# Kernel optimization log

Measured on AMD Instinct MI355X. Metric: run time of the kernel, lower is better.

Reference implementation:

```python
import jax, jax.numpy as jnp
import numpy as np


def _conv3x3(x, w):
    # x: [B,Cin,H,W], w: [Cout,Cin,3,3], stride 1, pad 1
    return jax.lax.conv_general_dilated(x, w, window_strides=(1, 1), padding='SAME',
                                        dimension_numbers=('NCHW', 'OIHW', 'NCHW'))


def _affine(x, s, b):
    # per-channel folded eval-mode BatchNorm (+ absorbed conv bias)
    return x * s[None, :, None, None] + b[None, :, None, None]


def _lif_encode(h, thr, beta, T=4):
    # LIF integrate-and-fire scan: membrane = beta*m + h; STE spike; soft reset.
    def step(m, _):
        m = beta * m + h
        sig = jax.nn.sigmoid(4.0 * (m - thr))
        hard = (m > thr).astype(h.dtype)
        spk = sig + jax.lax.stop_gradient(hard - sig)  # surrogate-gradient STE
        return m - spk * thr, spk
    _, spikes = jax.lax.scan(step, jnp.zeros_like(h), None, length=T)
    return spikes  # [T,B,C_bot,H,W]


def _level(feat, ew, ebs, ebb, thr, braw, dw, dbs, dbb):
    h = _affine(_conv3x3(feat, ew), ebs, ebb)
    spikes = _lif_encode(h, thr, jax.nn.sigmoid(braw))
    avg = spikes.mean(axis=0)  # ber=0.0 -> BSC channel is identity
    return jax.nn.silu(_affine(_conv3x3(avg, dw), dbs, dbb))


def _forward(feat3, enc3_w, enc3_bn_s, enc3_bn_b, enc3_thr, enc3_beta_raw, dec3_w, dec3_bn_s, dec3_bn_b,
             feat4, enc4_w, enc4_bn_s, enc4_bn_b, enc4_thr, enc4_beta_raw, dec4_w, dec4_bn_s, dec4_bn_b,
             feat5, enc5_w, enc5_bn_s, enc5_bn_b, enc5_thr, enc5_beta_raw, dec5_w, dec5_bn_s, dec5_bn_b):
    r3 = _level(feat3, enc3_w, enc3_bn_s, enc3_bn_b, enc3_thr, enc3_beta_raw, dec3_w, dec3_bn_s, dec3_bn_b)
    r4 = _level(feat4, enc4_w, enc4_bn_s, enc4_bn_b, enc4_thr, enc4_beta_raw, dec4_w, dec4_bn_s, dec4_bn_b)
    r5 = _level(feat5, enc5_w, enc5_bn_s, enc5_bn_b, enc5_thr, enc5_beta_raw, dec5_w, dec5_bn_s, dec5_bn_b)
    return (r3, r4, r5)


def setup_inputs() -> dict:
    key = jax.random.key(0)
    C_bot, B = 36, 16
    levels = {3: (64, 160), 4: (128, 80), 5: (256, 40)}
    inp = {}
    k = key
    for lvl, (c, s) in levels.items():
        k, k1, k2, k3 = jax.random.split(k, 4)
        inp[f'feat{lvl}'] = jax.random.normal(k1, (B, c, s, s), jnp.float32)
        inp[f'enc{lvl}_w'] = jax.random.normal(k2, (C_bot, c, 3, 3), jnp.float32) / np.float32(np.sqrt(9 * c))
        inp[f'enc{lvl}_bn_s'] = jnp.ones((C_bot,), jnp.float32)
        inp[f'enc{lvl}_bn_b'] = jnp.zeros((C_bot,), jnp.float32)
        inp[f'enc{lvl}_thr'] = jnp.ones((1, C_bot, 1, 1), jnp.float32)
        inp[f'enc{lvl}_beta_raw'] = jnp.full((1, C_bot, 1, 1), 2.2, jnp.float32)
        inp[f'dec{lvl}_w'] = jax.random.normal(k3, (c, C_bot, 3, 3), jnp.float32) / np.float32(np.sqrt(9 * C_bot))
        inp[f'dec{lvl}_bn_s'] = jnp.ones((c,), jnp.float32)
        inp[f'dec{lvl}_bn_b'] = jnp.zeros((c,), jnp.float32)
    return inp


def reference(feat3, enc3_w, enc3_bn_s, enc3_bn_b, enc3_thr, enc3_beta_raw, dec3_w, dec3_bn_s, dec3_bn_b,
              feat4, enc4_w, enc4_bn_s, enc4_bn_b, enc4_thr, enc4_beta_raw, dec4_w, dec4_bn_s, dec4_bn_b,
              feat5, enc5_w, enc5_bn_s, enc5_bn_b, enc5_thr, enc5_beta_raw, dec5_w, dec5_bn_s, dec5_bn_b):
    return _forward(feat3, enc3_w, enc3_bn_s, enc3_bn_b, enc3_thr, enc3_beta_raw, dec3_w, dec3_bn_s, dec3_bn_b,
                    feat4, enc4_w, enc4_bn_s, enc4_bn_b, enc4_thr, enc4_beta_raw, dec4_w, dec4_bn_s, dec4_bn_b,
                    feat5, enc5_w, enc5_bn_s, enc5_bn_b, enc5_thr, enc5_beta_raw, dec5_w, dec5_bn_s, dec5_bn_b)
```

## Files before the change

kernel.cpp:

```cpp
#include <hip/hip_runtime.h>
#include <hip/hip_bf16.h>

typedef __attribute__((ext_vector_type(8)))  short short8v;
typedef __attribute__((ext_vector_type(16))) float f32x16;
typedef __attribute__((ext_vector_type(4)))  int   int4v;

template<int CIN>
__global__ __launch_bounds__(256) void pack_we(
    const float* __restrict__ w, __hip_bfloat16* __restrict__ whi,
    __hip_bfloat16* __restrict__ wlo, int total)
{
    const int NCHUNK = CIN / 16;
    int idx = blockIdx.x * 256 + threadIdx.x;
    if (idx >= total) return;
    int m  = idx & 31;
    int h  = (idx >> 5) & 1;
    int s  = (idx >> 6) % 9;
    int c  = (idx / 576) % NCHUNK;
    int cg = idx / (576 * NCHUNK);
    int co = cg * 32 + m;
    unsigned short vh[8], vl[8];
    #pragma unroll
    for (int j = 0; j < 8; ++j) {
        int ci = c * 16 + h * 8 + j;
        float x = (co < 36) ? w[(long)co * CIN * 9 + ci * 9 + s] : 0.f;
        __hip_bfloat16 xh = __float2bfloat16(x);
        float rem = x - __bfloat162float(xh);
        __hip_bfloat16 xl = __float2bfloat16(rem);
        vh[j] = *(unsigned short*)&xh;
        vl[j] = *(unsigned short*)&xl;
    }
    *(int4v*)(whi + (long)idx * 8) = *(int4v*)vh;
    *(int4v*)(wlo + (long)idx * 8) = *(int4v*)vl;
}

template<int CIN, int PXB>
__global__ __launch_bounds__(256) void feat_hl(
    const float* __restrict__ f, __hip_bfloat16* __restrict__ fhl,
    int HW, int npx)
{
    const int NCHUNK = CIN / 16;
    __shared__ float t[CIN][PXB];
    const int p0 = blockIdx.x * PXB;

    for (int i = threadIdx.x; i < CIN * PXB; i += 256) {
        int ci = i / PXB, px = i % PXB;
        int p = p0 + px;
        float v = 0.f;
        if (p < npx) {
            int b = p / HW, r = p - b * HW;
            v = f[((long)b * CIN + ci) * HW + r];
        }
        t[ci][px] = v;
    }
    __syncthreads();

    for (int i = threadIdx.x; i < PXB * NCHUNK * 4; i += 256) {
        int q  = i & 3;
        int px = (i >> 2) % PXB;
        int c  = i / (4 * PXB);
        int p = p0 + px;
        if (p >= npx) continue;
        const bool lo = (q >= 2);
        const int ch0 = c * 16 + (q & 1) * 8;
        unsigned short v[8];
        #pragma unroll
        for (int j = 0; j < 8; ++j) {
            float x = t[ch0 + j][px];
            __hip_bfloat16 xh = __float2bfloat16(x);
            if (lo) {
                float rem = x - __bfloat162float(xh);
                xh = __float2bfloat16(rem);
            }
            v[j] = *(unsigned short*)&xh;
        }
        *(int4v*)(fhl + ((long)c * npx + p) * 32 + q * 8) = *(int4v*)v;
    }
}

template<int CIN>
__global__ __launch_bounds__(256) void enc_mfma_cl(
    const __hip_bfloat16* __restrict__ fhl,
    const __hip_bfloat16* __restrict__ whi,
    const __hip_bfloat16* __restrict__ wlo,
    const float* __restrict__ bn_s, const float* __restrict__ bn_b,
    const float* __restrict__ thr, const float* __restrict__ beta_raw,
    __hip_bfloat16* __restrict__ avg,
    int H, int W, int tiles_x)
{
    const int NCHUNK = CIN / 16;
    __shared__ __align__(16) short sbuf[324 * 48];
    short* hi_t = sbuf;
    short* lo_t = sbuf + 324 * 24;

    const int tid = threadIdx.x;
    const int b   = blockIdx.y;
    const int tx0 = (blockIdx.x % tiles_x) * 16;
    const int ty0 = (blockIdx.x / tiles_x) * 16;
    const long npx = (long)16 * H * W;

    const int lane = tid & 63;
    const int wv   = tid >> 6;
    const int h    = lane >> 5;
    const int n    = lane & 31;
    const int lx   = n & 15;
    const int ly0  = wv * 4 + (n >> 4);

    f32x16 acc[2][2];
    #pragma unroll
    for (int cg = 0; cg < 2; ++cg)
        #pragma unroll
        for (int pf = 0; pf < 2; ++pf)
            #pragma unroll
            for (int k = 0; k < 16; ++k) acc[cg][pf][k] = 0.f;

    const char* aph = (const char*)whi + h * 512 + n * 16;
    const char* apl = (const char*)wlo + h * 512 + n * 16;
    const long  cgstride = (long)NCHUNK * 9216;

    for (int c = 0; c < NCHUNK; ++c) {
        for (int i = tid; i < 1296; i += 256) {
            int p = i >> 2, q = i & 3;
            int hy = p / 18, hx = p - hy * 18;
            int gy = ty0 + hy - 1, gx = tx0 + hx - 1;
            int4v v = {0, 0, 0, 0};
            if (gy >= 0 && gy < H && gx >= 0 && gx < W) {
                long pg = (long)(b * H + gy) * W + gx;
                v = *(const int4v*)(fhl + ((long)c * npx + pg) * 32 + q * 8);
            }
            char* dst = (q < 2) ? (char*)hi_t + p * 48 + q * 16
                                : (char*)lo_t + p * 48 + (q - 2) * 16;
            *(int4v*)dst = v;
        }
        __syncthreads();

        const char* ahc = aph + (long)c * 9216;
        const char* alc = apl + (long)c * 9216;
        #pragma unroll
        for (int s = 0; s < 9; ++s) {
            const int dy = s / 3, dx = s % 3;
            const int p0 = (ly0 + dy) * 18 + (lx + dx);
            const int p1 = p0 + 36;
            short8v bh0 = *(const short8v*)((const char*)hi_t + p0 * 48 + h * 16);
            short8v bh1 = *(const short8v*)((const char*)hi_t + p1 * 48 + h * 16);
            short8v bl0 = *(const short8v*)((const char*)lo_t + p0 * 48 + h * 16);
            short8v bl1 = *(const short8v*)((const char*)lo_t + p1 * 48 + h * 16);
            #pragma unroll
            for (int cg = 0; cg < 2; ++cg) {
                short8v af = *(const short8v*)(ahc + cg * cgstride + s * 1024);
                short8v al = *(const short8v*)(alc + cg * cgstride + s * 1024);
                acc[cg][0] = __builtin_amdgcn_mfma_f32_32x32x16_bf16(af, bh0, acc[cg][0], 0, 0, 0);
                acc[cg][0] = __builtin_amdgcn_mfma_f32_32x32x16_bf16(af, bl0, acc[cg][0], 0, 0, 0);
                acc[cg][0] = __builtin_amdgcn_mfma_f32_32x32x16_bf16(al, bh0, acc[cg][0], 0, 0, 0);
                acc[cg][1] = __builtin_amdgcn_mfma_f32_32x32x16_bf16(af, bh1, acc[cg][1], 0, 0, 0);
                acc[cg][1] = __builtin_amdgcn_mfma_f32_32x32x16_bf16(af, bl1, acc[cg][1], 0, 0, 0);
                acc[cg][1] = __builtin_amdgcn_mfma_f32_32x32x16_bf16(al, bh1, acc[cg][1], 0, 0, 0);
            }
        }
        __syncthreads();
    }

    for (int i = tid; i < 1280; i += 256)
        *(int4v*)((char*)sbuf + i * 16) = (int4v){0, 0, 0, 0};
    __syncthreads();

    #pragma unroll
    for (int cg = 0; cg < 2; ++cg) {
        #pragma unroll
        for (int r = 0; r < 16; ++r) {
            const int co = (cg << 5) + (r & 3) + ((r >> 2) << 3) + (h << 2);
            if (co < 36) {
                const float sc   = bn_s[co], sb = bn_b[co];
                const float beta = 1.f / (1.f + expf(-beta_raw[co]));
                const float t    = thr[co];
                #pragma unroll
                for (int pf = 0; pf < 2; ++pf) {
                    const int ly = ly0 + pf * 2;
                    float hv = acc[cg][pf][r] * sc + sb;
                    float m = 0.f, c2 = 0.f;
                    #pragma unroll
                    for (int s4 = 0; s4 < 4; ++s4) {
                        m = beta * m + hv;
                        if (m > t) { c2 += 1.f; m -= t; }
                    }
                    __hip_bfloat16 ov = __float2bfloat16(c2 * 0.25f);
                    sbuf[(ly * 16 + lx) * 40 + co] = *(short*)&ov;
                }
            }
        }
    }
    __syncthreads();

    const long tilebase = ((long)(b * H + ty0) * W + tx0) * 40;
    for (int i = tid; i < 1280; i += 256) {
        int px = i / 5, u = i - px * 5;
        int py2 = px >> 4, px2 = px & 15;
        *(int4v*)(avg + tilebase + ((long)py2 * W + px2) * 40 + u * 8) =
            *(const int4v*)(sbuf + px * 40 + u * 8);
    }
}

template<int CIN, int CIPER>
__global__ __launch_bounds__(256) void enc_mfma_p(
    const __hip_bfloat16* __restrict__ fhl,
    const __hip_bfloat16* __restrict__ whi,
    const __hip_bfloat16* __restrict__ wlo,
    float* __restrict__ partial,
    int H, int W, int tiles_x)
{
    const int NCH_TOT = CIN / 16;
    const int NCH_PER = CIPER / 16;
    __shared__ __align__(16) short sbuf[324 * 48];
    short* hi_t = sbuf;
    short* lo_t = sbuf + 324 * 24;

    const int tid = threadIdx.x;
    const int b   = blockIdx.y;
    const int cis = blockIdx.z;
    const int tx0 = (blockIdx.x % tiles_x) * 16;
    const int ty0 = (blockIdx.x / tiles_x) * 16;
    const long npx = (long)16 * H * W;

    const int lane = tid & 63;
    const int wv   = tid >> 6;
    const int h    = lane >> 5;
    const int n    = lane & 31;
    const int lx   = n & 15;
    const int ly0  = wv * 4 + (n >> 4);

    f32x16 acc[2][2];
    #pragma unroll
    for (int cg = 0; cg < 2; ++cg)
        #pragma unroll
        for (int pf = 0; pf < 2; ++pf)
            #pragma unroll
            for (int k = 0; k < 16; ++k) acc[cg][pf][k] = 0.f;

    const char* aph = (const char*)whi + h * 512 + n * 16;
    const char* apl = (const char*)wlo + h * 512 + n * 16;
    const long  cgstride = (long)NCH_TOT * 9216;

    for (int c = 0; c < NCH_PER; ++c) {
        const int gc = cis * NCH_PER + c;
        for (int i = tid; i < 1296; i += 256) {
            int p = i >> 2, q = i & 3;
            int hy = p / 18, hx = p - hy * 18;
            int gy = ty0 + hy - 1, gx = tx0 + hx - 1;
            int4v v = {0, 0, 0, 0};
            if (gy >= 0 && gy < H && gx >= 0 && gx < W) {
                long pg = (long)(b * H + gy) * W + gx;
                v = *(const int4v*)(fhl + ((long)gc * npx + pg) * 32 + q * 8);
            }
            char* dst = (q < 2) ? (char*)hi_t + p * 48 + q * 16
                                : (char*)lo_t + p * 48 + (q - 2) * 16;
            *(int4v*)dst = v;
        }
        __syncthreads();

        const char* ahc = aph + (long)gc * 9216;
        const char* alc = apl + (long)gc * 9216;
        #pragma unroll
        for (int s = 0; s < 9; ++s) {
            const int dy = s / 3, dx = s % 3;
            const int p0 = (ly0 + dy) * 18 + (lx + dx);
            const int p1 = p0 + 36;
            short8v bh0 = *(const short8v*)((const char*)hi_t + p0 * 48 + h * 16);
            short8v bh1 = *(const short8v*)((const char*)hi_t + p1 * 48 + h * 16);
            short8v bl0 = *(const short8v*)((const char*)lo_t + p0 * 48 + h * 16);
            short8v bl1 = *(const short8v*)((const char*)lo_t + p1 * 48 + h * 16);
            #pragma unroll
            for (int cg = 0; cg < 2; ++cg) {
                short8v af = *(const short8v*)(ahc + cg * cgstride + s * 1024);
                short8v al = *(const short8v*)(alc + cg * cgstride + s * 1024);
                acc[cg][0] = __builtin_amdgcn_mfma_f32_32x32x16_bf16(af, bh0, acc[cg][0], 0, 0, 0);
                acc[cg][0] = __builtin_amdgcn_mfma_f32_32x32x16_bf16(af, bl0, acc[cg][0], 0, 0, 0);
                acc[cg][0] = __builtin_amdgcn_mfma_f32_32x32x16_bf16(al, bh0, acc[cg][0], 0, 0, 0);
                acc[cg][1] = __builtin_amdgcn_mfma_f32_32x32x16_bf16(af, bh1, acc[cg][1], 0, 0, 0);
                acc[cg][1] = __builtin_amdgcn_mfma_f32_32x32x16_bf16(af, bl1, acc[cg][1], 0, 0, 0);
                acc[cg][1] = __builtin_amdgcn_mfma_f32_32x32x16_bf16(al, bh1, acc[cg][1], 0, 0, 0);
            }
        }
        __syncthreads();
    }

    const int HW = H * W;
    const long total = (long)16 * 36 * HW;
    #pragma unroll
    for (int cg = 0; cg < 2; ++cg) {
        #pragma unroll
        for (int r = 0; r < 16; ++r) {
            const int co = (cg << 5) + (r & 3) + ((r >> 2) << 3) + (h << 2);
            if (co < 36) {
                #pragma unroll
                for (int pf = 0; pf < 2; ++pf) {
                    const int gy = ty0 + ly0 + pf * 2, gx = tx0 + lx;
                    if (gy < H && gx < W)
                        partial[(long)cis * total + ((long)(b * 36 + co) * HW + gy * W + gx)]
                            = acc[cg][pf][r];
                }
            }
        }
    }
}

template<int CIN, int CIPER, int CICHUNK, int COCHUNK, int TDIM, bool PARTIAL, bool CL>
__global__ __launch_bounds__(TDIM* TDIM) void enc_tiled(
    const float* __restrict__ feat,
    const float* __restrict__ w,
    const float* __restrict__ bn_s, const float* __restrict__ bn_b,
    const float* __restrict__ thr, const float* __restrict__ beta_raw,
    __hip_bfloat16* __restrict__ avg,
    float* __restrict__ partial,
    int H, int W, int tiles_x)
{
    const int TPB  = TDIM * TDIM;
    const int HALOD = TDIM + 2;
    const int NCO  = 36 / COCHUNK;
    __shared__ float fs[CICHUNK][HALOD][HALOD];

    const int tile = blockIdx.x;
    const int b    = blockIdx.y;
    const int coc  = blockIdx.z % NCO;
    const int cis  = blockIdx.z / NCO;
    const int co0  = coc * COCHUNK;
    const int tx0  = (tile % tiles_x) * TDIM;
    const int ty0  = (tile / tiles_x) * TDIM;

    const int tx = threadIdx.x % TDIM;
    const int ty = threadIdx.x / TDIM;
    const int ox = tx0 + tx, oy = ty0 + ty;

    float acc[COCHUNK];
    #pragma unroll
    for (int c = 0; c < COCHUNK; ++c) acc[c] = 0.f;

    const float* fb = feat + (long)b * CIN * H * W;
    const int ci_base = cis * CIPER;

    for (int cc = ci_base; cc < ci_base + CIPER; cc += CICHUNK) {
        for (int i = threadIdx.x; i < CICHUNK * HALOD * HALOD; i += TPB) {
            int ci = i / (HALOD * HALOD);
            int r  = i % (HALOD * HALOD);
            int hy = r / HALOD, hx = r % HALOD;
            int gy = ty0 + hy - 1, gx = tx0 + hx - 1;
            float v = 0.f;
            if (gy >= 0 && gy < H && gx >= 0 && gx < W)
                v = fb[((long)(cc + ci) * H + gy) * W + gx];
            fs[ci][hy][hx] = v;
        }
        __syncthreads();

        for (int ci = 0; ci < CICHUNK; ++ci) {
            float f0 = fs[ci][ty    ][tx], f1 = fs[ci][ty    ][tx+1], f2 = fs[ci][ty    ][tx+2];
            float f3 = fs[ci][ty + 1][tx], f4 = fs[ci][ty + 1][tx+1], f5 = fs[ci][ty + 1][tx+2];
            float f6 = fs[ci][ty + 2][tx], f7 = fs[ci][ty + 2][tx+1], f8 = fs[ci][ty + 2][tx+2];
            const float* wq = w + (long)(cc + ci) * 9;
            #pragma unroll
            for (int j = 0; j < COCHUNK; ++j) {
                const float* ww = wq + (long)(co0 + j) * CIN * 9;
                acc[j] += f0 * ww[0] + f1 * ww[1] + f2 * ww[2]
                        + f3 * ww[3] + f4 * ww[4] + f5 * ww[5]
                        + f6 * ww[6] + f7 * ww[7] + f8 * ww[8];
            }
        }
        __syncthreads();
    }

    if (ox < W && oy < H) {
        if (PARTIAL) {
            #pragma unroll
            for (int j = 0; j < COCHUNK; ++j)
                partial[((((long)cis * 16 + b) * 36 + (co0 + j)) * H + oy) * W + ox] = acc[j];
        } else {
            float cnt[COCHUNK];
            #pragma unroll
            for (int j = 0; j < COCHUNK; ++j) {
                int co = co0 + j;
                float hh   = acc[j] * bn_s[co] + bn_b[co];
                float beta = 1.f / (1.f + expf(-beta_raw[co]));
                float t    = thr[co];
                float m = 0.f, c2 = 0.f;
                #pragma unroll
                for (int s = 0; s < 4; ++s) {
                    m = beta * m + hh;
                    if (m > t) { c2 += 1.f; m -= t; }
                }
                cnt[j] = c2 * 0.25f;
            }
            if (CL) {
                unsigned* dp = (unsigned*)(avg + ((long)(b * H + oy) * W + ox) * 40 + co0);
                #pragma unroll
                for (int j2 = 0; j2 < COCHUNK / 2; ++j2) {
                    __hip_bfloat16 h0 = __float2bfloat16(cnt[2 * j2]);
                    __hip_bfloat16 h1 = __float2bfloat16(cnt[2 * j2 + 1]);
                    unsigned u0 = *(unsigned short*)&h0;
                    unsigned u1 = *(unsigned short*)&h1;
                    dp[j2] = u0 | (u1 << 16);
                }
            } else {
                #pragma unroll
                for (int j = 0; j < COCHUNK; ++j)
                    avg[(((long)b * 36 + (co0 + j)) * H + oy) * W + ox] = __float2bfloat16(cnt[j]);
            }
        }
    }
}

template<int SPLITS, bool CL>
__global__ __launch_bounds__(256) void combine_lif(
    const float* __restrict__ partial,
    const float* __restrict__ bn_s, const float* __restrict__ bn_b,
    const float* __restrict__ thr, const float* __restrict__ beta_raw,
    __hip_bfloat16* __restrict__ avg, int H, int W, int total)
{
    int idx = blockIdx.x * 256 + threadIdx.x;
    if (idx >= total) return;
    int HW = H * W;
    int co = (idx / HW) % 36;
    float hh = 0.f;
    #pragma unroll
    for (int s = 0; s < SPLITS; ++s) hh += partial[(long)s * total + idx];
    hh = hh * bn_s[co] + bn_b[co];
    float beta = 1.f / (1.f + expf(-beta_raw[co]));
    float t    = thr[co];
    float m = 0.f, cnt = 0.f;
    #pragma unroll
    for (int s = 0; s < 4; ++s) {
        m = beta * m + hh;
        if (m > t) { cnt += 1.f; m -= t; }
    }
    if (CL) {
        int b = idx / (36 * HW);
        int rem = idx % HW;
        int y = rem / W, x = rem % W;
        avg[((long)(b * H + y) * W + x) * 40 + co] = __float2bfloat16(cnt * 0.25f);
    } else {
        avg[idx] = __float2bfloat16(cnt * 0.25f);
    }
}

__global__ __launch_bounds__(256) void pack_w(
    const float* __restrict__ w, __hip_bfloat16* __restrict__ ap, int total)
{
    int idx = blockIdx.x * 256 + threadIdx.x;
    if (idx >= total) return;
    int m  = idx & 31;
    int h  = (idx >> 5) & 1;
    int s  = (idx >> 6) % 23;
    int cg = idx / (23 * 64);
    int o  = 2 * s + h;
    int co = cg * 32 + m;
    unsigned short v[8];
    #pragma unroll
    for (int j = 0; j < 8; ++j) {
        float x = 0.f;
        if (o < 45) {
            int tap = o / 5, oct = o % 5, ci = oct * 8 + j;
            if (ci < 36) x = w[(long)co * 324 + ci * 9 + tap];
        }
        __hip_bfloat16 hv = __float2bfloat16(x);
        v[j] = *(unsigned short*)&hv;
    }
    *(int4v*)(ap + (long)idx * 8) = *(int4v*)v;
}

template<int COG>
__global__ __launch_bounds__(256) void dec_mfma(
    const __hip_bfloat16* __restrict__ avg_cl,
    const __hip_bfloat16* __restrict__ apack,
    const float* __restrict__ bn_s, const float* __restrict__ bn_b,
    float* __restrict__ out, int Cout, int H, int W, int tiles_x)
{
    __shared__ __hip_bfloat16 tile[12960];

    const int tid    = threadIdx.x;
    const int b      = blockIdx.y;
    const int cgbase = blockIdx.z * COG;
    const int tx0 = (blockIdx.x % tiles_x) * 16;
    const int ty0 = (blockIdx.x / tiles_x) * 16;

    {
        const __hip_bfloat16* ab = avg_cl + (long)b * H * W * 40;
        for (int i = tid; i < 1620; i += 256) {
            int row = i / 90, u = i - row * 90;
            int px = u / 5, un = u - px * 5;
            int gy = ty0 + row - 1, gx = tx0 + px - 1;
            int4v v = {0, 0, 0, 0};
            if (gy >= 0 && gy < H && gx >= 0 && gx < W)
                v = *(const int4v*)(ab + ((long)gy * W + gx) * 40 + un * 8);
            *(int4v*)(tile + (row * 18 + px) * 40 + un * 8) = v;
        }
    }
    __syncthreads();

    const int lane = tid & 63;
    const int wv   = tid >> 6;
    const int h    = lane >> 5;
    const int n    = lane & 31;
    const int lx   = n & 15;
    const int ly0  = wv * 4 + (n >> 4);

    const char* tb  = (const char*)tile;
    const int   bb0 = ((ly0 + 1) * 18 + (lx + 1)) * 80;
    const int   bb1 = bb0 + 2 * 18 * 80;

    const char* ap = (const char*)apack + (long)cgbase * 23552 + h * 512 + n * 16;

    f32x16 acc[COG][2];
    #pragma unroll
    for (int cg = 0; cg < COG; ++cg)
        #pragma unroll
        for (int pf = 0; pf < 2; ++pf)
            #pragma unroll
            for (int k = 0; k < 16; ++k) acc[cg][pf][k] = 0.f;

    #pragma unroll
    for (int s = 0; s < 23; ++s) {
        int o0 = 2 * s;     if (o0 > 44) o0 = 44;
        int o1 = 2 * s + 1; if (o1 > 44) o1 = 44;
        const int C0 = ((o0 / 5) / 3 - 1) * 1440 + ((o0 / 5) % 3 - 1) * 80 + (o0 % 5) * 16;
        const int C1 = ((o1 / 5) / 3 - 1) * 1440 + ((o1 / 5) % 3 - 1) * 80 + (o1 % 5) * 16;
        const int offc = h ? C1 : C0;
        short8v bf0 = *(const short8v*)(tb + (bb0 + offc));
        short8v bf1 = *(const short8v*)(tb + (bb1 + offc));
        #pragma unroll
        for (int cg = 0; cg < COG; ++cg) {
            short8v af = *(const short8v*)(ap + cg * 23552 + s * 1024);
            acc[cg][0] = __builtin_amdgcn_mfma_f32_32x32x16_bf16(af, bf0, acc[cg][0], 0, 0, 0);
            acc[cg][1] = __builtin_amdgcn_mfma_f32_32x32x16_bf16(af, bf1, acc[cg][1], 0, 0, 0);
        }
    }

    #pragma unroll
    for (int cg = 0; cg < COG; ++cg) {
        #pragma unroll
        for (int r = 0; r < 16; ++r) {
            const int co = ((cgbase + cg) << 5) + (r & 3) + ((r >> 2) << 3) + (h << 2);
            const float sc = bn_s[co], bc = bn_b[co];
            #pragma unroll
            for (int pf = 0; pf < 2; ++pf) {
                const int ly = ly0 + pf * 2;
                const int gy = ty0 + ly, gx = tx0 + lx;
                float v = acc[cg][pf][r] * sc + bc;
                v = v / (1.f + __expf(-v));
                if (gy < H && gx < W)
                    out[(((long)b * Cout + co) * H + gy) * W + gx] = v;
            }
        }
    }
}

template<int COCHUNK, int TDIM>
__global__ __launch_bounds__(TDIM* TDIM) void dec_tiled(
    const __hip_bfloat16* __restrict__ avg,
    const float* __restrict__ w,
    const float* __restrict__ bn_s, const float* __restrict__ bn_b,
    float* __restrict__ out,
    int Cout, int H, int W, int tiles_x)
{
    const int CIN = 36;
    const int TPB = TDIM * TDIM;
    const int HALOD = TDIM + 2;
    __shared__ float fs[CIN][HALOD][HALOD];

    const int tile = blockIdx.x;
    const int b    = blockIdx.y;
    const int co0  = blockIdx.z * COCHUNK;
    const int tx0  = (tile % tiles_x) * TDIM;
    const int ty0  = (tile / tiles_x) * TDIM;

    const int tx = threadIdx.x % TDIM;
    const int ty = threadIdx.x / TDIM;
    const int ox = tx0 + tx, oy = ty0 + ty;

    const __hip_bfloat16* ab = avg + (long)b * CIN * H * W;

    for (int i = threadIdx.x; i < CIN * HALOD * HALOD; i += TPB) {
        int ci = i / (HALOD * HALOD);
        int r  = i % (HALOD * HALOD);
        int hy = r / HALOD, hx = r % HALOD;
        int gy = ty0 + hy - 1, gx = tx0 + hx - 1;
        float v = 0.f;
        if (gy >= 0 && gy < H && gx >= 0 && gx < W)
            v = __bfloat162float(ab[((long)ci * H + gy) * W + gx]);
        fs[ci][hy][hx] = v;
    }
    __syncthreads();

    float acc[COCHUNK];
    #pragma unroll
    for (int j = 0; j < COCHUNK; ++j) acc[j] = 0.f;

    for (int ci = 0; ci < CIN; ++ci) {
        float f0 = fs[ci][ty    ][tx], f1 = fs[ci][ty    ][tx+1], f2 = fs[ci][ty    ][tx+2];
        float f3 = fs[ci][ty + 1][tx], f4 = fs[ci][ty + 1][tx+1], f5 = fs[ci][ty + 1][tx+2];
        float f6 = fs[ci][ty + 2][tx], f7 = fs[ci][ty + 2][tx+1], f8 = fs[ci][ty + 2][tx+2];
        #pragma unroll
        for (int j = 0; j < COCHUNK; ++j) {
            const float* ww = w + ((long)(co0 + j) * CIN + ci) * 9;
            acc[j] += f0 * ww[0] + f1 * ww[1] + f2 * ww[2]
                    + f3 * ww[3] + f4 * ww[4] + f5 * ww[5]
                    + f6 * ww[6] + f7 * ww[7] + f8 * ww[8];
        }
    }

    if (ox < W && oy < H) {
        #pragma unroll
        for (int j = 0; j < COCHUNK; ++j) {
            int co = co0 + j;
            float v = acc[j] * bn_s[co] + bn_b[co];
            out[(((long)b * Cout + co) * H + oy) * W + ox] = v / (1.f + expf(-v));
        }
    }
}

extern "C" void kernel_launch(void* const* d_in, const int* in_sizes, int n_in,
                              void* d_out, int out_size, void* d_ws, size_t ws_size,
                              hipStream_t stream)
{
    const int B = 16;
    const int C[3] = {64, 128, 256};
    const int S[3] = {160, 80, 40};

    float* out = (float*)d_out;
    long out_off[3]; long off = 0;
    for (int l = 0; l < 3; ++l) { out_off[l] = off; off += (long)B * C[l] * S[l] * S[l]; }

    const long avgcl_bytes[3] = {32768000L, 8192000L, 2048000L};
    long avgcl_off[3]; long boff = 0;
    for (int l = 0; l < 3; ++l) { avgcl_off[l] = boff; boff += avgcl_bytes[l]; }
    const long avgcl_total = boff;
    const long ap_bytes[3] = {47104L, 94208L, 188416L};
    long ap_off[3];
    for (int l = 0; l < 3; ++l) { ap_off[l] = boff; boff += ap_bytes[l]; }
    const long we_bytes[3] = {73728L, 147456L, 294912L};
    long wehi_off[3], welo_off[3];
    for (int l = 0; l < 3; ++l) { wehi_off[l] = boff; boff += we_bytes[l];
                                  welo_off[l] = boff; boff += we_bytes[l]; }
    const long part5_off = boff;
    const long part5_bytes = 4L * B * 36 * 1600 * 4;
    boff += part5_bytes;
    const size_t need_full = (size_t)boff;
    const size_t need_min  = (size_t)part5_off;
    const long fhl_bytes[3] = {104857600L, 52428800L, 26214400L};
    long fhl_off[3];
    for (int l = 0; l < 2; ++l) { fhl_off[l] = boff; boff += fhl_bytes[l]; }
    const size_t need_cl = (size_t)boff;
    fhl_off[2] = boff; boff += fhl_bytes[2];
    const size_t need_cl5 = (size_t)boff;

    char* wsb = (char*)d_ws;

    if (ws_size >= need_min) {
        const bool split5  = ws_size >= need_full;
        const bool use_cl  = ws_size >= need_cl;
        const bool use_cl5 = ws_size >= need_cl5;
        hipMemsetAsync(wsb, 0, avgcl_total, stream);

        for (int l = 0; l < 3; ++l) {
            const float* dec_w = (const float*)d_in[9 * l + 6];
            int total = (C[l] / 32) * 23 * 2 * 32;
            pack_w<<<(total + 255) / 256, 256, 0, stream>>>(
                dec_w, (__hip_bfloat16*)(wsb + ap_off[l]), total);
        }
        {
            const float* enc_w3 = (const float*)d_in[1];
            int total = 2 * (64 / 16) * 9 * 2 * 32;
            pack_we<64><<<(total + 255) / 256, 256, 0, stream>>>(
                enc_w3, (__hip_bfloat16*)(wsb + wehi_off[0]),
                (__hip_bfloat16*)(wsb + welo_off[0]), total);
        }
        {
            const float* enc_w4 = (const float*)d_in[10];
            int total = 2 * (128 / 16) * 9 * 2 * 32;
            pack_we<128><<<(total + 255) / 256, 256, 0, stream>>>(
                enc_w4, (__hip_bfloat16*)(wsb + wehi_off[1]),
                (__hip_bfloat16*)(wsb + welo_off[1]), total);
        }
        if (use_cl5) {
            const float* enc_w5 = (const float*)d_in[19];
            int total = 2 * (256 / 16) * 9 * 2 * 32;
            pack_we<256><<<(total + 255) / 256, 256, 0, stream>>>(
                enc_w5, (__hip_bfloat16*)(wsb + wehi_off[2]),
                (__hip_bfloat16*)(wsb + welo_off[2]), total);
        }
        if (use_cl) {
            {
                int HW = 160 * 160, npx = B * HW;
                feat_hl<64, 64><<<(npx + 63) / 64, 256, 0, stream>>>(
                    (const float*)d_in[0], (__hip_bfloat16*)(wsb + fhl_off[0]), HW, npx);
            }
            {
                int HW = 80 * 80, npx = B * HW;
                feat_hl<128, 64><<<(npx + 63) / 64, 256, 0, stream>>>(
                    (const float*)d_in[9], (__hip_bfloat16*)(wsb + fhl_off[1]), HW, npx);
            }
        }
        if (use_cl5) {
            int HW = 40 * 40, npx = B * HW;
            feat_hl<256, 32><<<(npx + 31) / 32, 256, 0, stream>>>(
                (const float*)d_in[18], (__hip_bfloat16*)(wsb + fhl_off[2]), HW, npx);
        }

        for (int l = 0; l < 3; ++l) {
            const int base = 9 * l;
            const float* feat     = (const float*)d_in[base + 0];
            const float* enc_w    = (const float*)d_in[base + 1];
            const float* enc_bn_s = (const float*)d_in[base + 2];
            const float* enc_bn_b = (const float*)d_in[base + 3];
            const float* enc_thr  = (const float*)d_in[base + 4];
            const float* enc_beta = (const float*)d_in[base + 5];
            const float* dec_bn_s = (const float*)d_in[base + 7];
            const float* dec_bn_b = (const float*)d_in[base + 8];

            const int Hs = S[l], Wsz = S[l];
            __hip_bfloat16* avg_cl = (__hip_bfloat16*)(wsb + avgcl_off[l]);
            const __hip_bfloat16* ap = (const __hip_bfloat16*)(wsb + ap_off[l]);
            float* r = out + out_off[l];

            if (l == 0) {
                dim3 eg(100, B);
                if (use_cl)
                    enc_mfma_cl<64><<<eg, 256, 0, stream>>>(
                        (const __hip_bfloat16*)(wsb + fhl_off[0]),
                        (const __hip_bfloat16*)(wsb + wehi_off[0]),
                        (const __hip_bfloat16*)(wsb + welo_off[0]),
                        enc_bn_s, enc_bn_b, enc_thr, enc_beta, avg_cl, Hs, Wsz, 10);
                else
                    enc_tiled<64, 64, 16, 12, 16, false, true><<<dim3(100, B, 3), 256, 0, stream>>>(
                        feat, enc_w, enc_bn_s, enc_bn_b, enc_thr, enc_beta, avg_cl, nullptr, Hs, Wsz, 10);
                dim3 dg(100, B, 1);
                dec_mfma<2><<<dg, 256, 0, stream>>>(avg_cl, ap, dec_bn_s, dec_bn_b, r, 64, Hs, Wsz, 10);
            } else if (l == 1) {
                dim3 eg(25, B);
                if (use_cl)
                    enc_mfma_cl<128><<<eg, 256, 0, stream>>>(
                        (const __hip_bfloat16*)(wsb + fhl_off[1]),
                        (const __hip_bfloat16*)(wsb + wehi_off[1]),
                        (const __hip_bfloat16*)(wsb + welo_off[1]),
                        enc_bn_s, enc_bn_b, enc_thr, enc_beta, avg_cl, Hs, Wsz, 5);
                else
                    enc_tiled<128, 128, 16, 12, 16, false, true><<<dim3(25, B, 3), 256, 0, stream>>>(
                        feat, enc_w, enc_bn_s, enc_bn_b, enc_thr, enc_beta, avg_cl, nullptr, Hs, Wsz, 5);
                dim3 dg(25, B, 2);
                dec_mfma<2><<<dg, 256, 0, stream>>>(avg_cl, ap, dec_bn_s, dec_bn_b, r, 128, Hs, Wsz, 5);
            } else {
                if (use_cl5) {
                    float* partial5 = (float*)(wsb + part5_off);
                    dim3 eg(9, B, 4);
                    enc_mfma_p<256, 64><<<eg, 256, 0, stream>>>(
                        (const __hip_bfloat16*)(wsb + fhl_off[2]),
                        (const __hip_bfloat16*)(wsb + wehi_off[2]),
                        (const __hip_bfloat16*)(wsb + welo_off[2]),
                        partial5, Hs, Wsz, 3);
                    int total = B * 36 * Hs * Wsz;
                    combine_lif<4, true><<<(total + 255) / 256, 256, 0, stream>>>(
                        partial5, enc_bn_s, enc_bn_b, enc_thr, enc_beta, avg_cl, Hs, Wsz, total);
                } else if (split5) {
                    float* partial5 = (float*)(wsb + part5_off);
                    dim3 eg(25, B, 12);
                    enc_tiled<256, 64, 16, 12, 8, true, true><<<eg, 64, 0, stream>>>(
                        feat, enc_w, enc_bn_s, enc_bn_b, enc_thr, enc_beta, nullptr, partial5, Hs, Wsz, 5);
                    int total = B * 36 * Hs * Wsz;
                    combine_lif<4, true><<<(total + 255) / 256, 256, 0, stream>>>(
                        partial5, enc_bn_s, enc_bn_b, enc_thr, enc_beta, avg_cl, Hs, Wsz, total);
                } else {
                    dim3 eg(25, B, 3);
                    enc_tiled<256, 256, 16, 12, 8, false, true><<<eg, 64, 0, stream>>>(
                        feat, enc_w, enc_bn_s, enc_bn_b, enc_thr, enc_beta, avg_cl, nullptr, Hs, Wsz, 5);
                }
                dim3 dg(9, B, 4);
                dec_mfma<2><<<dg, 256, 0, stream>>>(avg_cl, ap, dec_bn_s, dec_bn_b, r, 256, Hs, Wsz, 3);
            }
        }
    } else {
        __hip_bfloat16* ws = (__hip_bfloat16*)d_ws;
        long avg_off2[3]; long eoff = 0;
        for (int l = 0; l < 3; ++l) { avg_off2[l] = eoff; eoff += (long)B * 36 * S[l] * S[l]; }
        float* partial5 = (float*)(ws + ((eoff + 7) & ~7L));
        const long part5f = 4L * B * 36 * 40 * 40;
        const size_t old_need = (size_t)((eoff + 7) & ~7L) * 2 + part5f * 4;
        const bool split5 = ws_size >= old_need;

        for (int l = 0; l < 3; ++l) {
            const int base = 9 * l;
            const float* feat     = (const float*)d_in[base + 0];
            const float* enc_w    = (const float*)d_in[base + 1];
            const float* enc_bn_s = (const float*)d_in[base + 2];
            const float* enc_bn_b = (const float*)d_in[base + 3];
            const float* enc_thr  = (const float*)d_in[base + 4];
            const float* enc_beta = (const float*)d_in[base + 5];
            const float* dec_w    = (const float*)d_in[base + 6];
            const float* dec_bn_s = (const float*)d_in[base + 7];
            const float* dec_bn_b = (const float*)d_in[base + 8];

            const int Hs = S[l], Wsz = S[l], Cl = C[l];
            __hip_bfloat16* avg = ws + avg_off2[l];
            float* r = out + out_off[l];

            if (l == 0) {
                dim3 eg(100, B, 3);
                enc_tiled<64, 64, 16, 12, 16, false, false><<<eg, 256, 0, stream>>>(
                    feat, enc_w, enc_bn_s, enc_bn_b, enc_thr, enc_beta, avg, nullptr, Hs, Wsz, 10);
                dim3 dg(100, B, 2);
                dec_tiled<32, 16><<<dg, 256, 0, stream>>>(avg, dec_w, dec_bn_s, dec_bn_b, r, Cl, Hs, Wsz, 10);
            } else if (l == 1) {
                dim3 eg(25, B, 3);
                enc_tiled<128, 128, 16, 12, 16, false, false><<<eg, 256, 0, stream>>>(
                    feat, enc_w, enc_bn_s, enc_bn_b, enc_thr, enc_beta, avg, nullptr, Hs, Wsz, 5);
                dim3 dg(25, B, 4);
                dec_tiled<32, 16><<<dg, 256, 0, stream>>>(avg, dec_w, dec_bn_s, dec_bn_b, r, Cl, Hs, Wsz, 5);
            } else {
                if (split5) {
                    dim3 eg(25, B, 12);
                    enc_tiled<256, 64, 16, 12, 8, true, false><<<eg, 64, 0, stream>>>(
                        feat, enc_w, enc_bn_s, enc_bn_b, enc_thr, enc_beta, nullptr, partial5, Hs, Wsz, 5);
                    int total = B * 36 * Hs * Wsz;
                    combine_lif<4, false><<<(total + 255) / 256, 256, 0, stream>>>(
                        partial5, enc_bn_s, enc_bn_b, enc_thr, enc_beta, avg, Hs, Wsz, total);
                } else {
                    dim3 eg(25, B, 3);
                    enc_tiled<256, 256, 16, 12, 8, false, false><<<eg, 64, 0, stream>>>(
                        feat, enc_w, enc_bn_s, enc_bn_b, enc_thr, enc_beta, avg, nullptr, Hs, Wsz, 5);
                }
                dim3 dg(25, B, 16);
                dec_tiled<16, 8><<<dg, 64, 0, stream>>>(avg, dec_w, dec_bn_s, dec_bn_b, r, Cl, Hs, Wsz, 5);
            }
        }
    }
}
```

Measured before the change: 581.8 us.

## Prefetch next channel chunk into registers during MFMA compute in encoder convs

The encoder conv kernels now load the next input channel chunk's halo tile from global memory into registers while the current chunk's MFMAs run. The registers are then written to LDS at the start of the next iteration, so global load latency overlaps with compute instead of stalling before each chunk. This costs 24 extra VGPRs per thread for the staging buffer, which may lower occupancy or cause spills on top of the 64 accumulator registers.

```diff
diff --git a/kernel.cpp b/kernel.cpp
--- a/kernel.cpp
+++ b/kernel.cpp
@@ -118,21 +118,51 @@
     const char* apl = (const char*)wlo + h * 512 + n * 16;
     const long  cgstride = (long)NCHUNK * 9216;
 
-    for (int c = 0; c < NCHUNK; ++c) {
-        for (int i = tid; i < 1296; i += 256) {
+    int4v rv[6];
+    #pragma unroll
+    for (int k = 0; k < 6; ++k) {
+        const int i = tid + k * 256;
+        rv[k] = (int4v){0, 0, 0, 0};
+        if (i < 1296) {
             int p = i >> 2, q = i & 3;
             int hy = p / 18, hx = p - hy * 18;
             int gy = ty0 + hy - 1, gx = tx0 + hx - 1;
-            int4v v = {0, 0, 0, 0};
             if (gy >= 0 && gy < H && gx >= 0 && gx < W) {
                 long pg = (long)(b * H + gy) * W + gx;
-                v = *(const int4v*)(fhl + ((long)c * npx + pg) * 32 + q * 8);
-            }
-            char* dst = (q < 2) ? (char*)hi_t + p * 48 + q * 16
-                                : (char*)lo_t + p * 48 + (q - 2) * 16;
-            *(int4v*)dst = v;
-        }
+                rv[k] = *(const int4v*)(fhl + (0 * npx + pg) * 32 + q * 8);
+            }
+        }
+    }
+
+    for (int c = 0; c < NCHUNK; ++c) {
         __syncthreads();
+        #pragma unroll
+        for (int k = 0; k < 6; ++k) {
+            const int i = tid + k * 256;
+            if (i < 1296) {
+                int p = i >> 2, q = i & 3;
+                char* dst = (q < 2) ? (char*)hi_t + p * 48 + q * 16
+                                    : (char*)lo_t + p * 48 + (q - 2) * 16;
+                *(int4v*)dst = rv[k];
+            }
+        }
+        __syncthreads();
+        if (c + 1 < NCHUNK) {
+            #pragma unroll
+            for (int k = 0; k < 6; ++k) {
+                const int i = tid + k * 256;
+                rv[k] = (int4v){0, 0, 0, 0};
+                if (i < 1296) {
+                    int p = i >> 2, q = i & 3;
+                    int hy = p / 18, hx = p - hy * 18;
+                    int gy = ty0 + hy - 1, gx = tx0 + hx - 1;
+                    if (gy >= 0 && gy < H && gx >= 0 && gx < W) {
+                        long pg = (long)(b * H + gy) * W + gx;
+                        rv[k] = *(const int4v*)(fhl + ((long)(c + 1) * npx + pg) * 32 + q * 8);
+                    }
+                }
+            }
+        }
 
         const char* ahc = aph + (long)c * 9216;
         const char* alc = apl + (long)c * 9216;
@@ -157,8 +187,8 @@
                 acc[cg][1] = __builtin_amdgcn_mfma_f32_32x32x16_bf16(al, bh1, acc[cg][1], 0, 0, 0);
             }
         }
-        __syncthreads();
-    }
+    }
+    __syncthreads();
 
     for (int i = tid; i < 1280; i += 256)
         *(int4v*)((char*)sbuf + i * 16) = (int4v){0, 0, 0, 0};
@@ -240,22 +270,52 @@
     const char* apl = (const char*)wlo + h * 512 + n * 16;
     const long  cgstride = (long)NCH_TOT * 9216;
 
-    for (int c = 0; c < NCH_PER; ++c) {
-        const int gc = cis * NCH_PER + c;
-        for (int i = tid; i < 1296; i += 256) {
+    int4v rv[6];
+    #pragma unroll
+    for (int k = 0; k < 6; ++k) {
+        const int i = tid + k * 256;
+        rv[k] = (int4v){0, 0, 0, 0};
+        if (i < 1296) {
             int p = i >> 2, q = i & 3;
             int hy = p / 18, hx = p - hy * 18;
             int gy = ty0 + hy - 1, gx = tx0 + hx - 1;
-            int4v v = {0, 0, 0, 0};
             if (gy >= 0 && gy < H && gx >= 0 && gx < W) {
                 long pg = (long)(b * H + gy) * W + gx;
-                v = *(const int4v*)(fhl + ((long)gc * npx + pg) * 32 + q * 8);
-            }
-            char* dst = (q < 2) ? (char*)hi_t + p * 48 + q * 16
-                                : (char*)lo_t + p * 48 + (q - 2) * 16;
-            *(int4v*)dst = v;
-        }
+                rv[k] = *(const int4v*)(fhl + ((long)(cis * NCH_PER) * npx + pg) * 32 + q * 8);
+            }
+        }
+    }
+
+    for (int c = 0; c < NCH_PER; ++c) {
+        const int gc = cis * NCH_PER + c;
         __syncthreads();
+        #pragma unroll
+        for (int k = 0; k < 6; ++k) {
+            const int i = tid + k * 256;
+            if (i < 1296) {
+                int p = i >> 2, q = i & 3;
+                char* dst = (q < 2) ? (char*)hi_t + p * 48 + q * 16
+                                    : (char*)lo_t + p * 48 + (q - 2) * 16;
+                *(int4v*)dst = rv[k];
+            }
+        }
+        __syncthreads();
+        if (c + 1 < NCH_PER) {
+            #pragma unroll
+            for (int k = 0; k < 6; ++k) {
+                const int i = tid + k * 256;
+                rv[k] = (int4v){0, 0, 0, 0};
+                if (i < 1296) {
+                    int p = i >> 2, q = i & 3;
+                    int hy = p / 18, hx = p - hy * 18;
+                    int gy = ty0 + hy - 1, gx = tx0 + hx - 1;
+                    if (gy >= 0 && gy < H && gx >= 0 && gx < W) {
+                        long pg = (long)(b * H + gy) * W + gx;
+                        rv[k] = *(const int4v*)(fhl + ((long)(gc + 1) * npx + pg) * 32 + q * 8);
+                    }
+                }
+            }
+        }
 
         const char* ahc = aph + (long)gc * 9216;
         const char* alc = apl + (long)gc * 9216;
@@ -280,7 +340,6 @@
                 acc[cg][1] = __builtin_amdgcn_mfma_f32_32x32x16_bf16(al, bh1, acc[cg][1], 0, 0, 0);
             }
         }
-        __syncthreads();
     }
 
     const int HW = H * W;
```

New measurement: 571.1 us, median of 2. No clear change (-1.8%).

## Double-buffer LDS halo tiles with register prefetch in MFMA encoder kernels

Applied to the files above, without the earlier changes.

Each encoder MFMA kernel now keeps two LDS buffers for the input halo tile. The next chunk's global loads are issued into registers before the current chunk's MFMAs run. This overlaps global memory latency with matrix compute and cuts one barrier per chunk. In exchange, LDS use doubles to about 62 KB per block, which may lower occupancy, and each thread holds six extra vector registers.

```diff
diff --git a/kernel.cpp b/kernel.cpp
--- a/kernel.cpp
+++ b/kernel.cpp
@@ -89,9 +89,7 @@
     int H, int W, int tiles_x)
 {
     const int NCHUNK = CIN / 16;
-    __shared__ __align__(16) short sbuf[324 * 48];
-    short* hi_t = sbuf;
-    short* lo_t = sbuf + 324 * 24;
+    __shared__ __align__(16) short sbuf[2][324 * 48];
 
     const int tid = threadIdx.x;
     const int b   = blockIdx.y;
@@ -118,21 +116,44 @@
     const char* apl = (const char*)wlo + h * 512 + n * 16;
     const long  cgstride = (long)NCHUNK * 9216;
 
+    int4v rv[6];
+
+#define ENC_LOAD_CHUNK(CC)                                                  \
+    _Pragma("unroll")                                                       \
+    for (int k = 0; k < 6; ++k) {                                           \
+        const int i = tid + k * 256;                                        \
+        rv[k] = (int4v){0, 0, 0, 0};                                        \
+        if (i < 1296) {                                                     \
+            int p = i >> 2, q = i & 3;                                      \
+            int hy = p / 18, hx = p - hy * 18;                              \
+            int gy = ty0 + hy - 1, gx = tx0 + hx - 1;                       \
+            if (gy >= 0 && gy < H && gx >= 0 && gx < W) {                   \
+                long pg = (long)(b * H + gy) * W + gx;                      \
+                rv[k] = *(const int4v*)(fhl + ((long)(CC) * npx + pg) * 32 + q * 8); \
+            }                                                               \
+        }                                                                   \
+    }
+
+#define ENC_WRITE_BUF(BUF)                                                  \
+    _Pragma("unroll")                                                       \
+    for (int k = 0; k < 6; ++k) {                                           \
+        const int i = tid + k * 256;                                        \
+        if (i < 1296) {                                                     \
+            int p = i >> 2, q = i & 3;                                      \
+            char* dst = (q < 2) ? (char*)(BUF) + p * 48 + q * 16            \
+                                : (char*)((BUF) + 324 * 24) + p * 48 + (q - 2) * 16; \
+            *(int4v*)dst = rv[k];                                           \
+        }                                                                   \
+    }
+
+    ENC_LOAD_CHUNK(0);
+    ENC_WRITE_BUF(sbuf[0]);
+    if (NCHUNK > 1) { ENC_LOAD_CHUNK(1); }
+    __syncthreads();
+
     for (int c = 0; c < NCHUNK; ++c) {
-        for (int i = tid; i < 1296; i += 256) {
-            int p = i >> 2, q = i & 3;
-            int hy = p / 18, hx = p - hy * 18;
-            int gy = ty0 + hy - 1, gx = tx0 + hx - 1;
-            int4v v = {0, 0, 0, 0};
-            if (gy >= 0 && gy < H && gx >= 0 && gx < W) {
-                long pg = (long)(b * H + gy) * W + gx;
-                v = *(const int4v*)(fhl + ((long)c * npx + pg) * 32 + q * 8);
-            }
-            char* dst = (q < 2) ? (char*)hi_t + p * 48 + q * 16
-                                : (char*)lo_t + p * 48 + (q - 2) * 16;
-            *(int4v*)dst = v;
-        }
-        __syncthreads();
+        const short* hi_t = sbuf[c & 1];
+        const short* lo_t = hi_t + 324 * 24;
 
         const char* ahc = aph + (long)c * 9216;
         const char* alc = apl + (long)c * 9216;
@@ -157,11 +178,19 @@
                 acc[cg][1] = __builtin_amdgcn_mfma_f32_32x32x16_bf16(al, bh1, acc[cg][1], 0, 0, 0);
             }
         }
-        __syncthreads();
-    }
-
+
+        if (c + 1 < NCHUNK) {
+            short* nb = sbuf[(c + 1) & 1];
+            ENC_WRITE_BUF(nb);
+            if (c + 2 < NCHUNK) { ENC_LOAD_CHUNK(c + 2); }
+            __syncthreads();
+        }
+    }
+    __syncthreads();
+
+    short* ob = sbuf[0];
     for (int i = tid; i < 1280; i += 256)
-        *(int4v*)((char*)sbuf + i * 16) = (int4v){0, 0, 0, 0};
+        *(int4v*)((char*)ob + i * 16) = (int4v){0, 0, 0, 0};
     __syncthreads();
 
     #pragma unroll
@@ -184,7 +213,7 @@
                         if (m > t) { c2 += 1.f; m -= t; }
                     }
                     __hip_bfloat16 ov = __float2bfloat16(c2 * 0.25f);
-                    sbuf[(ly * 16 + lx) * 40 + co] = *(short*)&ov;
+                    ob[(ly * 16 + lx) * 40 + co] = *(short*)&ov;
                 }
             }
         }
@@ -196,8 +225,10 @@
         int px = i / 5, u = i - px * 5;
         int py2 = px >> 4, px2 = px & 15;
         *(int4v*)(avg + tilebase + ((long)py2 * W + px2) * 40 + u * 8) =
-            *(const int4v*)(sbuf + px * 40 + u * 8);
-    }
+            *(const int4v*)(ob + px * 40 + u * 8);
+    }
+#undef ENC_LOAD_CHUNK
+#undef ENC_WRITE_BUF
 }
 
 template<int CIN, int CIPER>
@@ -210,9 +241,7 @@
 {
     const int NCH_TOT = CIN / 16;
     const int NCH_PER = CIPER / 16;
-    __shared__ __align__(16) short sbuf[324 * 48];
-    short* hi_t = sbuf;
-    short* lo_t = sbuf + 324 * 24;
+    __shared__ __align__(16) short sbuf[2][324 * 48];
 
     const int tid = threadIdx.x;
     const int b   = blockIdx.y;
@@ -240,22 +269,45 @@
     const char* apl = (const char*)wlo + h * 512 + n * 16;
     const long  cgstride = (long)NCH_TOT * 9216;
 
+    int4v rv[6];
+
+#define ENC_LOAD_CHUNK_P(CC)                                                \
+    _Pragma("unroll")                                                       \
+    for (int k = 0; k < 6; ++k) {                                           \
+        const int i = tid + k * 256;                                        \
+        rv[k] = (int4v){0, 0, 0, 0};                                        \
+        if (i < 1296) {                                                     \
+            int p = i >> 2, q = i & 3;                                      \
+            int hy = p / 18, hx = p - hy * 18;                              \
+            int gy = ty0 + hy - 1, gx = tx0 + hx - 1;                       \
+            if (gy >= 0 && gy < H && gx >= 0 && gx < W) {                   \
+                long pg = (long)(b * H + gy) * W + gx;                      \
+                rv[k] = *(const int4v*)(fhl + ((long)(CC) * npx + pg) * 32 + q * 8); \
+            }                                                               \
+        }                                                                   \
+    }
+
+#define ENC_WRITE_BUF_P(BUF)                                                \
+    _Pragma("unroll")                                                       \
+    for (int k = 0; k < 6; ++k) {                                           \
+        const int i = tid + k * 256;                                        \
+        if (i < 1296) {                                                     \
+            int p = i >> 2, q = i & 3;                                      \
+            char* dst = (q < 2) ? (char*)(BUF) + p * 48 + q * 16            \
+                                : (char*)((BUF) + 324 * 24) + p * 48 + (q - 2) * 16; \
+            *(int4v*)dst = rv[k];                                           \
+        }                                                                   \
+    }
+
+    ENC_LOAD_CHUNK_P(cis * NCH_PER);
+    ENC_WRITE_BUF_P(sbuf[0]);
+    if (NCH_PER > 1) { ENC_LOAD_CHUNK_P(cis * NCH_PER + 1); }
+    __syncthreads();
+
     for (int c = 0; c < NCH_PER; ++c) {
         const int gc = cis * NCH_PER + c;
-        for (int i = tid; i < 1296; i += 256) {
-            int p = i >> 2, q = i & 3;
-            int hy = p / 18, hx = p - hy * 18;
-            int gy = ty0 + hy - 1, gx = tx0 + hx - 1;
-            int4v v = {0, 0, 0, 0};
-            if (gy >= 0 && gy < H && gx >= 0 && gx < W) {
-                long pg = (long)(b * H + gy) * W + gx;
-                v = *(const int4v*)(fhl + ((long)gc * npx + pg) * 32 + q * 8);
-            }
-            char* dst = (q < 2) ? (char*)hi_t + p * 48 + q * 16
-                                : (char*)lo_t + p * 48 + (q - 2) * 16;
-            *(int4v*)dst = v;
-        }
-        __syncthreads();
+        const short* hi_t = sbuf[c & 1];
+        const short* lo_t = hi_t + 324 * 24;
 
         const char* ahc = aph + (long)gc * 9216;
         const char* alc = apl + (long)gc * 9216;
@@ -280,7 +332,13 @@
                 acc[cg][1] = __builtin_amdgcn_mfma_f32_32x32x16_bf16(al, bh1, acc[cg][1], 0, 0, 0);
             }
         }
-        __syncthreads();
+
+        if (c + 1 < NCH_PER) {
+            short* nb = sbuf[(c + 1) & 1];
+            ENC_WRITE_BUF_P(nb);
+            if (c + 2 < NCH_PER) { ENC_LOAD_CHUNK_P(gc + 2); }
+            __syncthreads();
+        }
     }
 
     const int HW = H * W;
@@ -301,6 +359,8 @@
             }
         }
     }
+#undef ENC_LOAD_CHUNK_P
+#undef ENC_WRITE_BUF_P
 }
 
 template<int CIN, int CIPER, int CICHUNK, int COCHUNK, int TDIM, bool PARTIAL, bool CL>
```

Measured after the change: 582.0 us. No clear change (+0.0%).
